# Optimization experiments

Hardware: AMD Instinct MI355X
Metric: run time of the kernel (lower is better)

The kernel has to match this reference:

```python
import jax, jax.numpy as jnp
import numpy as np

N = 100000   # nodes
D = 8        # in_dim/2 (per-node phase dim)
H = 256      # hidden_dim
E = 1600000  # directed edges (avg degree 16)


def setup_inputs() -> dict:
    key = jax.random.key(0)
    ks = jax.random.split(key, 8)
    q = jax.random.normal(ks[0], (N, D), jnp.float32)
    p = jax.random.normal(ks[1], (N, D), jnp.float32)
    # per-node diagonal positive-definite mass matrix (what get_mass() produces:
    # diag(relu(diag(.)) + 1e-4)); keep it well-conditioned for the inverse.
    m_diag = jax.random.uniform(ks[2], (N, D), jnp.float32) + 0.5
    M = jax.vmap(jnp.diag)(m_diag)  # [N, D, D]
    src = jax.random.randint(ks[3], (E,), 0, N, dtype=jnp.int32)
    off = jax.random.randint(ks[4], (E,), 1, N, dtype=jnp.int32)
    dst = ((src + off) % N).astype(jnp.int32)  # guaranteed no self-edges (euclid>0)
    W1 = jax.random.normal(ks[5], (D, H), jnp.float32) / jnp.sqrt(D)
    b1 = jnp.zeros((H,), jnp.float32)
    W2 = jax.random.normal(ks[6], (H, D), jnp.float32) / jnp.sqrt(H)
    b2 = jnp.zeros((D,), jnp.float32)
    gravity = jnp.ones((1, 1), jnp.float32)
    return {"q": q, "p": p, "M": M, "src": src, "dst": dst,
            "W1": W1, "b1": b1, "W2": W2, "b2": b2, "gravity": gravity}


def _gcn(x, src, dst, norm_src, norm_dst, W, b, n_nodes):
    # DGL GraphConv norm='both': D_out^{-1/2} on src, sum-aggregate, D_in^{-1/2} on dst
    m = (x * norm_src[:, None])[src]                       # [E, F]
    agg = jax.ops.segment_sum(m, dst, num_segments=n_nodes)
    return (agg * norm_dst[:, None]) @ W + b


def reference(q, p, M, src, dst, W1, b1, W2, b2, gravity):
    n = q.shape[0]
    ones_e = jnp.ones(src.shape[0], q.dtype)
    out_deg = jax.ops.segment_sum(ones_e, src, num_segments=n)
    in_deg = jax.ops.segment_sum(ones_e, dst, num_segments=n)
    norm_src = jnp.where(out_deg > 0, out_deg, 1.0) ** -0.5
    norm_dst = jnp.where(in_deg > 0, in_deg, 1.0) ** -0.5

    def P_scalar(qq):
        # ConvGNN: GraphConv -> ReLU -> GraphConv, residual add
        h = jax.nn.relu(_gcn(qq, src, dst, norm_src, norm_dst, W1, b1, n))
        h = _gcn(h, src, dst, norm_src, norm_dst, W2, b2, n) + qq      # [N, D]
        euclid = jnp.linalg.norm(h[src] - h[dst], axis=-1)             # [E]
        masses = M[src] * M[dst]                                       # [E, D, D]
        return 0.5 * jnp.sum(gravity[0, 0] * masses / euclid[:, None, None])

    # dHdq = grad of potential P w.r.t q (torch.autograd.grad in original)
    dHdQ = jax.grad(P_scalar)(q)
    # dHdp: per-node p_i @ inv(M_i)  (self-loop graph, degree 1 per node)
    dHdP = jnp.linalg.solve(jnp.swapaxes(M, -1, -2), p[..., None])[..., 0]
    return jnp.concatenate([dHdQ, dHdP], axis=-1)  # [N, 2D]
```

## Files before the change

kernel.cpp:

```cpp
#include <hip/hip_runtime.h>
#include <hip/hip_fp16.h>

#define DD 8
#define HH 256
#define CH 8192
#define PAYBITS 17
#define PAYMASK 0x1FFFF
#define WHPITCH 12


typedef _Float16 h2f __attribute__((ext_vector_type(2)));

static __device__ __forceinline__ float2 u2f(unsigned w) {
    __half2 h = __builtin_bit_cast(__half2, w);
    return __half22float2(h);
}
static __device__ __forceinline__ float dot2u(unsigned w, h2f z, float c) {
#if __has_builtin(__builtin_amdgcn_fdot2)
    return __builtin_amdgcn_fdot2(__builtin_bit_cast(h2f, w), z, c, false);
#else
    float2 f = u2f(w);
    return fmaf(f.y, (float)z[1], fmaf(f.x, (float)z[0], c));
#endif
}
static __device__ __forceinline__ h2f pkh(float a, float b) {
    h2f r; r[0] = (_Float16)a; r[1] = (_Float16)b; return r;
}


__global__ void k_coarse(const int* __restrict__ src, const int* __restrict__ dst,
                         int* __restrict__ gHistIn, int* __restrict__ gHistOut,
                         int NB, int E) {
    __shared__ int hIn[256], hOut[256];
    if (threadIdx.x < 256) { hIn[threadIdx.x] = 0; hOut[threadIdx.x] = 0; }
    __syncthreads();
    int lo = blockIdx.x * CH;
    int hi = min(lo + CH, E);
    for (int i = lo + threadIdx.x; i < hi; i += blockDim.x) {
        atomicAdd(&hIn[dst[i] >> 9], 1);
        atomicAdd(&hOut[src[i] >> 9], 1);
    }
    __syncthreads();
    if (threadIdx.x < NB) {
        int ci = hIn[threadIdx.x], co = hOut[threadIdx.x];
        if (ci) atomicAdd(&gHistIn[threadIdx.x], ci);
        if (co) atomicAdd(&gHistOut[threadIdx.x], co);
    }
}

__global__ void k_cscan(const int* __restrict__ gHistIn, const int* __restrict__ gHistOut,
                        int* __restrict__ cStartIn, int* __restrict__ cStartOut,
                        int* __restrict__ cCurIn, int* __restrict__ cCurOut,
                        int NB, int E) {
    __shared__ int s[256];
#pragma unroll
    for (int dir = 0; dir < 2; dir++) {
        const int* gh = dir ? gHistOut : gHistIn;
        int* cs = dir ? cStartOut : cStartIn;
        int* cc = dir ? cCurOut : cCurIn;
        int v = (threadIdx.x < NB) ? gh[threadIdx.x] : 0;
        s[threadIdx.x] = v;
        __syncthreads();
        for (int off = 1; off < 256; off <<= 1) {
            int t = (threadIdx.x >= off) ? s[threadIdx.x - off] : 0;
            __syncthreads();
            s[threadIdx.x] += t;
            __syncthreads();
        }
        if (threadIdx.x < NB) {
            int ex = s[threadIdx.x] - v;
            cs[threadIdx.x] = ex;
            cc[threadIdx.x] = ex;
        }
        if (threadIdx.x == 0) cs[NB] = E;
        __syncthreads();
    }
}

__global__ void k_part2(const int* __restrict__ src, const int* __restrict__ dst,
                        int* __restrict__ cCurIn, int* __restrict__ cCurOut,
                        int* __restrict__ P_in, int* __restrict__ P_out,
                        int NB, int E) {
    int dir = blockIdx.y;
    const int* key = dir ? src : dst;
    const int* pay = dir ? dst : src;
    int* cCur = dir ? cCurOut : cCurIn;
    int* P    = dir ? P_out   : P_in;
    __shared__ int h[256];
    if (threadIdx.x < 256) h[threadIdx.x] = 0;
    __syncthreads();
    int lo = blockIdx.x * CH;
    int hi = min(lo + CH, E);
    for (int i = lo + threadIdx.x; i < hi; i += blockDim.x)
        atomicAdd(&h[key[i] >> 9], 1);
    __syncthreads();
    if (threadIdx.x < NB) {
        int c = h[threadIdx.x];
        h[threadIdx.x] = c ? atomicAdd(&cCur[threadIdx.x], c) : 0;
    }
    __syncthreads();
    for (int i = lo + threadIdx.x; i < hi; i += blockDim.x) {
        int k = key[i];
        int pos = atomicAdd(&h[k >> 9], 1);
        P[pos] = ((k & 511) << PAYBITS) | pay[i];
    }
}

__launch_bounds__(512)
__global__ void k_fine2(const int* __restrict__ cStartIn, const int* __restrict__ cStartOut,
                        const int* __restrict__ P_in, const int* __restrict__ P_out,
                        int* __restrict__ start_in, int* __restrict__ start_out,
                        int* __restrict__ csr_in, int* __restrict__ csr_out, int N) {
    int dir = blockIdx.y;
    const int* cStart = dir ? cStartOut : cStartIn;
    const int* P      = dir ? P_out     : P_in;
    int* start        = dir ? start_out : start_in;
    int* csr          = dir ? csr_out   : csr_in;
    __shared__ int cnt[512], scn[512];
    int b = blockIdx.x;
    int lo = cStart[b], hi = cStart[b + 1];
    cnt[threadIdx.x] = 0;
    __syncthreads();
    for (int i = lo + threadIdx.x; i < hi; i += 512)
        atomicAdd(&cnt[P[i] >> PAYBITS], 1);
    __syncthreads();
    int own = cnt[threadIdx.x];
    scn[threadIdx.x] = own;
    __syncthreads();
    for (int off = 1; off < 512; off <<= 1) {
        int t = (threadIdx.x >= off) ? scn[threadIdx.x - off] : 0;
        __syncthreads();
        scn[threadIdx.x] += t;
        __syncthreads();
    }
    int base = lo + scn[threadIdx.x] - own;
    int node = (b << 9) + threadIdx.x;
    if (node < N) start[node] = base;
    cnt[threadIdx.x] = base;
    __syncthreads();
    for (int i = lo + threadIdx.x; i < hi; i += 512) {
        int p = P[i];
        int pos = atomicAdd(&cnt[p >> PAYBITS], 1);
        csr[pos] = p & PAYMASK;
    }
}

__global__ void k_prep(const float* __restrict__ q, const float* __restrict__ p,
                       const float* __restrict__ M,
                       const float* __restrict__ W1, const float* __restrict__ W2,
                       unsigned* __restrict__ W12h,
                       int* __restrict__ start_in, int* __restrict__ start_out,
                       float* __restrict__ a, float* __restrict__ b,
                       __half2* __restrict__ hm, __half* __restrict__ qn,
                       float* __restrict__ out, int N, int E) {
    int t = blockIdx.x * blockDim.x + threadIdx.x;
    if (t == 0) { start_in[N] = E; start_out[N] = E; }
    if (t < HH * 8) {
        int j = t >> 3, k = t & 7;
        __half2 hh;
        if (k < 4) {
            hh.x = __float2half(W1[(2 * k) * HH + j]);
            hh.y = __float2half(W1[(2 * k + 1) * HH + j]);
            W12h[j * WHPITCH + k] = *(unsigned*)&hh;
        } else {
            int kk = k - 4;
            hh.x = __float2half(W2[j * DD + 2 * kk]);
            hh.y = __float2half(W2[j * DD + 2 * kk + 1]);
            W12h[j * WHPITCH + 4 + kk] = *(unsigned*)&hh;
        }
    }
    int v = t;
    if (v >= N) return;
    int ei1 = (v + 1 < N) ? start_in[v + 1]  : E;
    int eo1 = (v + 1 < N) ? start_out[v + 1] : E;
    float din  = (float)(ei1 - start_in[v]);
    float dout = (float)(eo1 - start_out[v]);
    float av = 1.0f / sqrtf(dout > 0.f ? dout : 1.f);
    float bv = 1.0f / sqrtf(din  > 0.f ? din  : 1.f);
    a[v] = av; b[v] = bv;
#pragma unroll
    for (int d = 0; d < DD; d++) {
        float m = M[(size_t)v * DD * DD + d * (DD + 1)];
        __half2 hmv;
        hmv.x = __float2half(0.f);
        hmv.y = __float2half(m);
        hm[(size_t)v * DD + d] = hmv;
        qn[(size_t)v * DD + d] = __float2half(av * q[(size_t)v * DD + d]);
        out[(size_t)v * 2 * DD + DD + d] = p[(size_t)v * DD + d] / m;
    }
}

static __device__ __forceinline__
void acc_h8(uint4 r, float acc[8]) {
    float2 f;
    f = __half22float2(*(__half2*)&r.x); acc[0] += f.x; acc[1] += f.y;
    f = __half22float2(*(__half2*)&r.y); acc[2] += f.x; acc[3] += f.y;
    f = __half22float2(*(__half2*)&r.z); acc[4] += f.x; acc[5] += f.y;
    f = __half22float2(*(__half2*)&r.w); acc[6] += f.x; acc[7] += f.y;
}

static __device__ __forceinline__
void unpack_hm(uint4 r0, uint4 r1, float h[8], float m[8]) {
    float2 f;
    f = __half22float2(*(__half2*)&r0.x); h[0] = f.x; m[0] = f.y;
    f = __half22float2(*(__half2*)&r0.y); h[1] = f.x; m[1] = f.y;
    f = __half22float2(*(__half2*)&r0.z); h[2] = f.x; m[2] = f.y;
    f = __half22float2(*(__half2*)&r0.w); h[3] = f.x; m[3] = f.y;
    f = __half22float2(*(__half2*)&r1.x); h[4] = f.x; m[4] = f.y;
    f = __half22float2(*(__half2*)&r1.y); h[5] = f.x; m[5] = f.y;
    f = __half22float2(*(__half2*)&r1.z); h[6] = f.x; m[6] = f.y;
    f = __half22float2(*(__half2*)&r1.w); h[7] = f.x; m[7] = f.y;
}

static __device__ __forceinline__
void gather_h8(const int* __restrict__ csr, const __half* __restrict__ x,
               int e, int e1, float acc[8]) {
    for (; e + 3 < e1; e += 4) {
        int u0 = csr[e], u1 = csr[e + 1], u2 = csr[e + 2], u3 = csr[e + 3];
        uint4 r0 = *(const uint4*)(x + (size_t)u0 * DD);
        uint4 r1 = *(const uint4*)(x + (size_t)u1 * DD);
        uint4 r2 = *(const uint4*)(x + (size_t)u2 * DD);
        uint4 r3 = *(const uint4*)(x + (size_t)u3 * DD);
        acc_h8(r0, acc); acc_h8(r1, acc); acc_h8(r2, acc); acc_h8(r3, acc);
    }
    for (; e < e1; e++) {
        uint4 r = *(const uint4*)(x + (size_t)csr[e] * DD);
        acc_h8(r, acc);
    }
}

__launch_bounds__(256)
__global__ void k_agg_mlp_fwd(const int* __restrict__ start, const int* __restrict__ csr,
                              const __half* __restrict__ qn,
                              const float* __restrict__ a, const float* __restrict__ b,
                              const unsigned* __restrict__ W12h, const float* __restrict__ b1,
                              float* __restrict__ agg1, __half* __restrict__ ya, int N) {
    __shared__ unsigned sWH[HH * WHPITCH];
    __shared__ float sb1[HH];
    for (int i = threadIdx.x; i < HH * WHPITCH; i += 256) sWH[i] = W12h[i];
    for (int i = threadIdx.x; i < HH; i += 256) sb1[i] = b1[i];
    __syncthreads();
    int t = blockIdx.x * 256 + threadIdx.x;
    int v = t >> 4, l16 = t & 15, sub = (t >> 3) & 1, d = t & 7;
    if (v >= N) return;
    int e0 = start[v], e1 = start[v + 1];
    float ag[DD] = {0.f, 0.f, 0.f, 0.f, 0.f, 0.f, 0.f, 0.f};
    for (int e = e0 + l16; e < e1; e += 16) {
        uint4 r = *(const uint4*)(qn + (size_t)csr[e] * DD);
        acc_h8(r, ag);
    }
#pragma unroll
    for (int m = 1; m < 16; m <<= 1)
#pragma unroll
        for (int k = 0; k < DD; k++) ag[k] += __shfl_xor(ag[k], m);
    if (l16 < 2) {
        float4 val = l16 ? make_float4(ag[4], ag[5], ag[6], ag[7])
                         : make_float4(ag[0], ag[1], ag[2], ag[3]);
        ((float4*)(agg1 + (size_t)v * DD))[l16] = val;
    }
    float bv = b[v];
    h2f zh[4];
#pragma unroll
    for (int k = 0; k < 4; k++) zh[k] = pkh(bv * ag[2 * k], bv * ag[2 * k + 1]);
    float acc[DD] = {0.f, 0.f, 0.f, 0.f, 0.f, 0.f, 0.f, 0.f};
    for (int c = 0; c < HH / 16; c += 2) {
        int j0 = (c << 4) | l16, j1 = j0 + 16;
        const uint4* r0 = (const uint4*)(sWH + j0 * WHPITCH);
        const uint4* r1 = (const uint4*)(sWH + j1 * WHPITCH);
        uint4 w1a = r0[0], w2a = r0[1];
        uint4 w1b = r1[0], w2b = r1[1];
        float u0 = sb1[j0], u1 = sb1[j1];
        u0 = dot2u(w1a.x, zh[0], u0); u0 = dot2u(w1a.y, zh[1], u0);
        u0 = dot2u(w1a.z, zh[2], u0); u0 = dot2u(w1a.w, zh[3], u0);
        u1 = dot2u(w1b.x, zh[0], u1); u1 = dot2u(w1b.y, zh[1], u1);
        u1 = dot2u(w1b.z, zh[2], u1); u1 = dot2u(w1b.w, zh[3], u1);
        float h0 = fmaxf(u0, 0.f);
        float h1 = fmaxf(u1, 0.f);
        float2 f;
        f = u2f(w2a.x); acc[0] = fmaf(h0, f.x, acc[0]); acc[1] = fmaf(h0, f.y, acc[1]);
        f = u2f(w2a.y); acc[2] = fmaf(h0, f.x, acc[2]); acc[3] = fmaf(h0, f.y, acc[3]);
        f = u2f(w2a.z); acc[4] = fmaf(h0, f.x, acc[4]); acc[5] = fmaf(h0, f.y, acc[5]);
        f = u2f(w2a.w); acc[6] = fmaf(h0, f.x, acc[6]); acc[7] = fmaf(h0, f.y, acc[7]);
        f = u2f(w2b.x); acc[0] = fmaf(h1, f.x, acc[0]); acc[1] = fmaf(h1, f.y, acc[1]);
        f = u2f(w2b.y); acc[2] = fmaf(h1, f.x, acc[2]); acc[3] = fmaf(h1, f.y, acc[3]);
        f = u2f(w2b.z); acc[4] = fmaf(h1, f.x, acc[4]); acc[5] = fmaf(h1, f.y, acc[5]);
        f = u2f(w2b.w); acc[6] = fmaf(h1, f.x, acc[6]); acc[7] = fmaf(h1, f.y, acc[7]);
    }
#pragma unroll
    for (int m = 1; m < 16; m <<= 1)
#pragma unroll
        for (int k = 0; k < DD; k++) acc[k] += __shfl_xor(acc[k], m);
    float yl = acc[0];
#pragma unroll
    for (int k = 1; k < DD; k++) yl = (d == k) ? acc[k] : yl;
    if (!sub) ya[(size_t)v * DD + d] = __float2half(a[v] * yl);
}

__launch_bounds__(256)
__global__ void k_h_node(const int* __restrict__ start, const int* __restrict__ csr,
                         const __half* __restrict__ ya, const float* __restrict__ b,
                         const float* __restrict__ q, const float* __restrict__ b2,
                         __half2* __restrict__ hm, int N) {
    int t = blockIdx.x * 256 + threadIdx.x;
    int v = t >> 1, half = t & 1;
    if (v >= N) return;
    int e0 = start[v], e1 = start[v + 1];
    int mid = e0 + ((e1 - e0) >> 1);
    float acc[8] = {0.f, 0.f, 0.f, 0.f, 0.f, 0.f, 0.f, 0.f};
    gather_h8(csr, ya, half ? mid : e0, half ? e1 : mid, acc);
#pragma unroll
    for (int k = 0; k < 8; k++) acc[k] += __shfl_xor(acc[k], 1);
    if (!half) {
        float bv = b[v];
        const float4* qp = (const float4*)(q + (size_t)v * DD);
        float4 q0 = qp[0], q1 = qp[1];
        float hq[8] = {q0.x, q0.y, q0.z, q0.w, q1.x, q1.y, q1.z, q1.w};
        __half2* hp = hm + (size_t)v * DD;
#pragma unroll
        for (int k = 0; k < DD; k++) {
            float hval = fmaf(bv, acc[k], b2[k] + hq[k]);
            __half2 cur = hp[k];
            cur.x = __float2half(hval);
            hp[k] = cur;
        }
    }
}

__launch_bounds__(256)
__global__ void k_gh4(const int* __restrict__ start_in, const int* __restrict__ csr_in,
                      const int* __restrict__ start_out, const int* __restrict__ csr_out,
                      const __half2* __restrict__ hm,
                      const float* __restrict__ b, const float* __restrict__ grav,
                      float* __restrict__ gh, __half* __restrict__ bgh, int N) {
    int t = blockIdx.x * 256 + threadIdx.x;
    int v = t >> 2, sub = t & 3, dir = sub >> 1, half = sub & 1;
    if (v >= N) return;
    const uint4* srec = (const uint4*)(hm + (size_t)v * DD);
    uint4 s0 = srec[0], s1 = srec[1];
    float hv[8], mv[8];
    unpack_hm(s0, s1, hv, mv);
    const int* start = dir ? start_out : start_in;
    const int* csr   = dir ? csr_out   : csr_in;
    int e0 = start[v], e1 = start[v + 1];
    int mid = e0 + ((e1 - e0) >> 1);
    int e = half ? mid : e0, hi = half ? e1 : mid;
    float coef = -0.5f * grav[0];
    float acc[8] = {0.f, 0.f, 0.f, 0.f, 0.f, 0.f, 0.f, 0.f};
    for (; e + 1 < hi; e += 2) {
        int u0 = csr[e], u1 = csr[e + 1];
        const uint4* r0p = (const uint4*)(hm + (size_t)u0 * DD);
        const uint4* r1p = (const uint4*)(hm + (size_t)u1 * DD);
        uint4 x0 = r0p[0], x1 = r0p[1], y0 = r1p[0], y1 = r1p[1];
        float hu0[8], mu0[8], hu1[8], mu1[8];
        unpack_hm(x0, x1, hu0, mu0);
        unpack_hm(y0, y1, hu1, mu1);
        float d0[8], d1[8];
        float e20 = 0.f, S0 = 0.f, e21 = 0.f, S1 = 0.f;
#pragma unroll
        for (int k = 0; k < 8; k++) {
            d0[k] = hv[k] - hu0[k];
            d1[k] = hv[k] - hu1[k];
            e20 = fmaf(d0[k], d0[k], e20);
            e21 = fmaf(d1[k], d1[k], e21);
            S0 = fmaf(mv[k], mu0[k], S0);
            S1 = fmaf(mv[k], mu1[k], S1);
        }
        float r0 = rsqrtf(e20), r1 = rsqrtf(e21);
        float c0 = coef * S0 * r0 * r0 * r0;
        float c1 = coef * S1 * r1 * r1 * r1;
#pragma unroll
        for (int k = 0; k < 8; k++)
            acc[k] = fmaf(c0, d0[k], fmaf(c1, d1[k], acc[k]));
    }
    if (e < hi) {
        int u = csr[e];
        const uint4* rp = (const uint4*)(hm + (size_t)u * DD);
        uint4 x0 = rp[0], x1 = rp[1];
        float hu[8], mu[8];
        unpack_hm(x0, x1, hu, mu);
        float df[8];
        float e2 = 0.f, S = 0.f;
#pragma unroll
        for (int k = 0; k < 8; k++) {
            df[k] = hv[k] - hu[k];
            e2 = fmaf(df[k], df[k], e2);
            S = fmaf(mv[k], mu[k], S);
        }
        float r = rsqrtf(e2);
        float c = coef * S * r * r * r;
#pragma unroll
        for (int k = 0; k < 8; k++) acc[k] = fmaf(c, df[k], acc[k]);
    }
#pragma unroll
    for (int k = 0; k < 8; k++) acc[k] += __shfl_xor(acc[k], 1);
#pragma unroll
    for (int k = 0; k < 8; k++) acc[k] += __shfl_xor(acc[k], 2);
    if (sub == 0) {
        float4* gp = (float4*)(gh + (size_t)v * DD);
        gp[0] = make_float4(acc[0], acc[1], acc[2], acc[3]);
        gp[1] = make_float4(acc[4], acc[5], acc[6], acc[7]);
        float bv = b[v];
        __half2* bp = (__half2*)(bgh + (size_t)v * DD);
        bp[0] = __floats2half2_rn(bv * acc[0], bv * acc[1]);
        bp[1] = __floats2half2_rn(bv * acc[2], bv * acc[3]);
        bp[2] = __floats2half2_rn(bv * acc[4], bv * acc[5]);
        bp[3] = __floats2half2_rn(bv * acc[6], bv * acc[7]);
    }
}

__launch_bounds__(256)
__global__ void k_bgh_mlp_bwd(const int* __restrict__ start, const int* __restrict__ csr,
                              const __half* __restrict__ bgh,
                              const float* __restrict__ agg1,
                              const float* __restrict__ a, const float* __restrict__ b,
                              const unsigned* __restrict__ W12h, const float* __restrict__ b1,
                              __half* __restrict__ gz1b, int N) {
    __shared__ unsigned sWH[HH * WHPITCH];
    __shared__ float sb1[HH];
    for (int i = threadIdx.x; i < HH * WHPITCH; i += 256) sWH[i] = W12h[i];
    for (int i = threadIdx.x; i < HH; i += 256) sb1[i] = b1[i];
    __syncthreads();
    int t = blockIdx.x * 256 + threadIdx.x;
    int v = t >> 4, l16 = t & 15, sub = (t >> 3) & 1, d = t & 7;
    if (v >= N) return;
    int e0 = start[v], e1 = start[v + 1];
    float gq[DD] = {0.f, 0.f, 0.f, 0.f, 0.f, 0.f, 0.f, 0.f};
    for (int e = e0 + l16; e < e1; e += 16) {
        uint4 r = *(const uint4*)(bgh + (size_t)csr[e] * DD);
        acc_h8(r, gq);
    }
#pragma unroll
    for (int m = 1; m < 16; m <<= 1)
#pragma unroll
        for (int k = 0; k < DD; k++) gq[k] += __shfl_xor(gq[k], m);
    float bv = b[v], av = a[v];
    float zl = bv * agg1[(size_t)v * DD + d];
    h2f zh[4], gqh[4];
#pragma unroll
    for (int k = 0; k < 4; k++) {
        float za = __shfl(zl, 2 * k, 16), zb = __shfl(zl, 2 * k + 1, 16);
        zh[k] = pkh(za, zb);
        gqh[k] = pkh(gq[2 * k], gq[2 * k + 1]);
    }
    float gz[DD] = {0.f, 0.f, 0.f, 0.f, 0.f, 0.f, 0.f, 0.f};
    for (int c = 0; c < HH / 16; c += 2) {
        int j0 = (c << 4) | l16, j1 = j0 + 16;
        const uint4* r0 = (const uint4*)(sWH + j0 * WHPITCH);
        const uint4* r1 = (const uint4*)(sWH + j1 * WHPITCH);
        uint4 w1a = r0[0], w2a = r0[1];
        uint4 w1b = r1[0], w2b = r1[1];
        float u0 = sb1[j0], u1 = sb1[j1];
        u0 = dot2u(w1a.x, zh[0], u0); u0 = dot2u(w1a.y, zh[1], u0);
        u0 = dot2u(w1a.z, zh[2], u0); u0 = dot2u(w1a.w, zh[3], u0);
        u1 = dot2u(w1b.x, zh[0], u1); u1 = dot2u(w1b.y, zh[1], u1);
        u1 = dot2u(w1b.z, zh[2], u1); u1 = dot2u(w1b.w, zh[3], u1);
        float ga0 = dot2u(w2a.x, gqh[0], 0.f);
        ga0 = dot2u(w2a.y, gqh[1], ga0);
        ga0 = dot2u(w2a.z, gqh[2], ga0);
        ga0 = dot2u(w2a.w, gqh[3], ga0);
        float ga1 = dot2u(w2b.x, gqh[0], 0.f);
        ga1 = dot2u(w2b.y, gqh[1], ga1);
        ga1 = dot2u(w2b.z, gqh[2], ga1);
        ga1 = dot2u(w2b.w, gqh[3], ga1);
        float g0 = (u0 > 0.f) ? av * ga0 : 0.f;
        float g1 = (u1 > 0.f) ? av * ga1 : 0.f;
        float2 f;
        f = u2f(w1a.x); gz[0] = fmaf(g0, f.x, gz[0]); gz[1] = fmaf(g0, f.y, gz[1]);
        f = u2f(w1a.y); gz[2] = fmaf(g0, f.x, gz[2]); gz[3] = fmaf(g0, f.y, gz[3]);
        f = u2f(w1a.z); gz[4] = fmaf(g0, f.x, gz[4]); gz[5] = fmaf(g0, f.y, gz[5]);
        f = u2f(w1a.w); gz[6] = fmaf(g0, f.x, gz[6]); gz[7] = fmaf(g0, f.y, gz[7]);
        f = u2f(w1b.x); gz[0] = fmaf(g1, f.x, gz[0]); gz[1] = fmaf(g1, f.y, gz[1]);
        f = u2f(w1b.y); gz[2] = fmaf(g1, f.x, gz[2]); gz[3] = fmaf(g1, f.y, gz[3]);
        f = u2f(w1b.z); gz[4] = fmaf(g1, f.x, gz[4]); gz[5] = fmaf(g1, f.y, gz[5]);
        f = u2f(w1b.w); gz[6] = fmaf(g1, f.x, gz[6]); gz[7] = fmaf(g1, f.y, gz[7]);
    }
#pragma unroll
    for (int m = 1; m < 16; m <<= 1)
#pragma unroll
        for (int k = 0; k < DD; k++) gz[k] += __shfl_xor(gz[k], m);
    float out_l = gz[0];
#pragma unroll
    for (int k = 1; k < DD; k++) out_l = (d == k) ? gz[k] : out_l;
    if (!sub) gz1b[(size_t)v * DD + d] = __float2half(bv * out_l);
}

__launch_bounds__(256)
__global__ void k_out_node(const int* __restrict__ start, const int* __restrict__ csr,
                           const __half* __restrict__ gz1b, const float* __restrict__ gh,
                           const float* __restrict__ a, float* __restrict__ out, int N) {
    int t = blockIdx.x * 256 + threadIdx.x;
    int v = t >> 1, half = t & 1;
    if (v >= N) return;
    int e0 = start[v], e1 = start[v + 1];
    int mid = e0 + ((e1 - e0) >> 1);
    float acc[8] = {0.f, 0.f, 0.f, 0.f, 0.f, 0.f, 0.f, 0.f};
    gather_h8(csr, gz1b, half ? mid : e0, half ? e1 : mid, acc);
#pragma unroll
    for (int k = 0; k < 8; k++) acc[k] += __shfl_xor(acc[k], 1);
    if (!half) {
        float av = a[v];
        const float4* gp = (const float4*)(gh + (size_t)v * DD);
        float4 g0 = gp[0], g1 = gp[1];
        float4* op = (float4*)(out + (size_t)v * 2 * DD);
        op[0] = make_float4(fmaf(av, acc[0], g0.x), fmaf(av, acc[1], g0.y),
                            fmaf(av, acc[2], g0.z), fmaf(av, acc[3], g0.w));
        op[1] = make_float4(fmaf(av, acc[4], g1.x), fmaf(av, acc[5], g1.y),
                            fmaf(av, acc[6], g1.z), fmaf(av, acc[7], g1.w));
    }
}


extern "C" void kernel_launch(void* const* d_in, const int* in_sizes, int n_in,
                              void* d_out, int out_size, void* d_ws, size_t ws_size,
                              hipStream_t stream) {
    const float* q    = (const float*)d_in[0];
    const float* p    = (const float*)d_in[1];
    const float* M    = (const float*)d_in[2];
    const int*   src  = (const int*)d_in[3];
    const int*   dst  = (const int*)d_in[4];
    const float* W1   = (const float*)d_in[5];
    const float* b1   = (const float*)d_in[6];
    const float* W2   = (const float*)d_in[7];
    const float* b2   = (const float*)d_in[8];
    const float* grav = (const float*)d_in[9];
    float* out = (float*)d_out;

    int N = in_sizes[0] / DD;
    int E = in_sizes[3];
    size_t n = (size_t)N;
    int NB = (N + 511) >> 9;

    float*   ws   = (float*)d_ws;
    float*   a_   = ws;
    float*   b_   = ws + n;
    __half*  qn   = (__half*)(ws + 2 * n);
    float*   agg1 = ws + 10 * n;
    float*   gh   = ws + 18 * n;
    __half2* hm   = (__half2*)(ws + 26 * n);
    __half*  ya   = (__half*)(ws + 34 * n);
    __half*  bgh  = (__half*)(ws + 38 * n);
    __half*  gz1b = (__half*)(ws + 42 * n);

    int* iw        = (int*)(ws + 46 * n);
    int* csr_in    = iw;
    int* csr_out   = iw + (size_t)E;
    int* start_in  = iw + 2 * (size_t)E;
    int* start_out = start_in + n + 1;
    int* gHistIn   = start_out + n + 1;
    int* gHistOut  = gHistIn + 256;
    int* cStartIn  = gHistOut + 256;
    int* cStartOut = cStartIn + NB + 1;
    int* cCurIn    = cStartOut + NB + 1;
    int* cCurOut   = cCurIn + NB;
    int* iwEnd     = cCurOut + NB;
    unsigned* W12h = (unsigned*)iwEnd;
    int* intAfter  = (int*)(W12h + HH * WHPITCH);
    int* P_in  = (E <= 16 * (long long)n) ? (int*)ws            : intAfter;
    int* P_out = (E <= 16 * (long long)n) ? (int*)(ws + 16 * n) : intAfter + E;

    hipMemsetAsync(gHistIn, 0, 512 * sizeof(int), stream);

    const int tb = 256;
    int gbN  = (N + tb - 1) / tb;
    int gb2  = (2 * N + tb - 1) / tb;
    int gb4  = (4 * N + tb - 1) / tb;
    int gb16 = (int)((16 * n + tb - 1) / tb);
    int gbC  = (E + CH - 1) / CH;

    k_coarse  <<<gbC, tb, 0, stream>>>(src, dst, gHistIn, gHistOut, NB, E);
    k_cscan   <<<1, 256, 0, stream>>>(gHistIn, gHistOut, cStartIn, cStartOut,
                                      cCurIn, cCurOut, NB, E);
    k_part2   <<<dim3(gbC, 2), tb, 0, stream>>>(src, dst, cCurIn, cCurOut,
                                                P_in, P_out, NB, E);
    k_fine2   <<<dim3(NB, 2), 512, 0, stream>>>(cStartIn, cStartOut, P_in, P_out,
                                                start_in, start_out, csr_in, csr_out, N);
    k_prep    <<<gbN, tb, 0, stream>>>(q, p, M, W1, W2, W12h, start_in, start_out,
                                       a_, b_, hm, qn, out, N, E);

    k_agg_mlp_fwd<<<gb16, tb, 0, stream>>>(start_in, csr_in, qn, a_, b_,
                                           W12h, b1, agg1, ya, N);
    k_h_node  <<<gb2, tb, 0, stream>>>(start_in, csr_in, ya, b_, q, b2, hm, N);
    k_gh4     <<<gb4, tb, 0, stream>>>(start_in, csr_in, start_out, csr_out,
                                       hm, b_, grav, gh, bgh, N);
    k_bgh_mlp_bwd<<<gb16, tb, 0, stream>>>(start_out, csr_out, bgh, agg1, a_, b_,
                                           W12h, b1, gz1b, N);
    k_out_node<<<gb2, tb, 0, stream>>>(start_out, csr_out, gz1b, gh, a_, out, N);
}
```

Before: 328.5 us.

## Repack MLP weights into per-lane fp16 pairs, use dot2 for second layer and DPP reductions

```diff
diff --git a/kernel.cpp b/kernel.cpp
--- a/kernel.cpp
+++ b/kernel.cpp
@@ -6,25 +6,54 @@
 #define CH 8192
 #define PAYBITS 17
 #define PAYMASK 0x1FFFF
-#define WHPITCH 12
+#define FPITCH 20
+#define BPITCH 28
 
 
 typedef _Float16 h2f __attribute__((ext_vector_type(2)));
 
-static __device__ __forceinline__ float2 u2f(unsigned w) {
-    __half2 h = __builtin_bit_cast(__half2, w);
-    return __half22float2(h);
-}
 static __device__ __forceinline__ float dot2u(unsigned w, h2f z, float c) {
 #if __has_builtin(__builtin_amdgcn_fdot2)
     return __builtin_amdgcn_fdot2(__builtin_bit_cast(h2f, w), z, c, false);
 #else
-    float2 f = u2f(w);
+    __half2 h = __builtin_bit_cast(__half2, w);
+    float2 f = __half22float2(h);
     return fmaf(f.y, (float)z[1], fmaf(f.x, (float)z[0], c));
 #endif
 }
 static __device__ __forceinline__ h2f pkh(float a, float b) {
     h2f r; r[0] = (_Float16)a; r[1] = (_Float16)b; return r;
+}
+static __device__ __forceinline__ unsigned pk2(float a, float b) {
+    __half2 hh; hh.x = __float2half(a); hh.y = __float2half(b);
+    return *(unsigned*)&hh;
+}
+
+template <int CTRL>
+static __device__ __forceinline__ float dppadd(float x) {
+    int y = __builtin_amdgcn_update_dpp(0, __builtin_bit_cast(int, x),
+                                        CTRL, 0xF, 0xF, true);
+    return x + __builtin_bit_cast(float, y);
+}
+static __device__ __forceinline__ void red16(float a[8]) {
+#pragma unroll
+    for (int k = 0; k < 8; k++) a[k] = dppadd<0xB1>(a[k]);
+#pragma unroll
+    for (int k = 0; k < 8; k++) a[k] = dppadd<0x4E>(a[k]);
+#pragma unroll
+    for (int k = 0; k < 8; k++) a[k] = dppadd<0x141>(a[k]);
+#pragma unroll
+    for (int k = 0; k < 8; k++) a[k] = dppadd<0x140>(a[k]);
+}
+static __device__ __forceinline__ void red2(float a[8]) {
+#pragma unroll
+    for (int k = 0; k < 8; k++) a[k] = dppadd<0xB1>(a[k]);
+}
+static __device__ __forceinline__ void red4(float a[8]) {
+#pragma unroll
+    for (int k = 0; k < 8; k++) a[k] = dppadd<0xB1>(a[k]);
+#pragma unroll
+    for (int k = 0; k < 8; k++) a[k] = dppadd<0x4E>(a[k]);
 }
 
 
@@ -148,26 +177,36 @@
 __global__ void k_prep(const float* __restrict__ q, const float* __restrict__ p,
                        const float* __restrict__ M,
                        const float* __restrict__ W1, const float* __restrict__ W2,
-                       unsigned* __restrict__ W12h,
+                       unsigned* __restrict__ Fp, unsigned* __restrict__ Bp,
                        int* __restrict__ start_in, int* __restrict__ start_out,
                        float* __restrict__ a, float* __restrict__ b,
                        __half2* __restrict__ hm, __half* __restrict__ qn,
                        float* __restrict__ out, int N, int E) {
     int t = blockIdx.x * blockDim.x + threadIdx.x;
     if (t == 0) { start_in[N] = E; start_out[N] = E; }
-    if (t < HH * 8) {
-        int j = t >> 3, k = t & 7;
-        __half2 hh;
-        if (k < 4) {
-            hh.x = __float2half(W1[(2 * k) * HH + j]);
-            hh.y = __float2half(W1[(2 * k + 1) * HH + j]);
-            W12h[j * WHPITCH + k] = *(unsigned*)&hh;
-        } else {
-            int kk = k - 4;
-            hh.x = __float2half(W2[j * DD + 2 * kk]);
-            hh.y = __float2half(W2[j * DD + 2 * kk + 1]);
-            W12h[j * WHPITCH + 4 + kk] = *(unsigned*)&hh;
+    if (t < 128) {
+        int ci = t >> 4, l16 = t & 15;
+        int j0 = ci * 32 + l16, j1 = j0 + 16;
+        unsigned* F = Fp + t * FPITCH;
+        unsigned* B = Bp + t * BPITCH;
+#pragma unroll
+        for (int k = 0; k < 4; k++) {
+            unsigned c0 = pk2(W1[(2 * k) * HH + j0], W1[(2 * k + 1) * HH + j0]);
+            unsigned c1 = pk2(W1[(2 * k) * HH + j1], W1[(2 * k + 1) * HH + j1]);
+            F[k] = c0; F[4 + k] = c1; B[k] = c0; B[4 + k] = c1;
         }
+#pragma unroll
+        for (int k = 0; k < 8; k++)
+            F[8 + k] = pk2(W2[j0 * DD + k], W2[j1 * DD + k]);
+#pragma unroll
+        for (int kk = 0; kk < 4; kk++) {
+            B[8 + kk]  = pk2(W2[j0 * DD + 2 * kk], W2[j0 * DD + 2 * kk + 1]);
+            B[12 + kk] = pk2(W2[j1 * DD + 2 * kk], W2[j1 * DD + 2 * kk + 1]);
+        }
+#pragma unroll
+        for (int d = 0; d < 8; d++)
+            B[16 + d] = pk2(W1[d * HH + j0], W1[d * HH + j1]);
+        B[24] = 0; B[25] = 0; B[26] = 0; B[27] = 0;
     }
     int v = t;
     if (v >= N) return;
@@ -233,11 +272,11 @@
 __global__ void k_agg_mlp_fwd(const int* __restrict__ start, const int* __restrict__ csr,
                               const __half* __restrict__ qn,
                               const float* __restrict__ a, const float* __restrict__ b,
-                              const unsigned* __restrict__ W12h, const float* __restrict__ b1,
+                              const unsigned* __restrict__ Fp, const float* __restrict__ b1,
                               float* __restrict__ agg1, __half* __restrict__ ya, int N) {
-    __shared__ unsigned sWH[HH * WHPITCH];
+    __shared__ unsigned sF[128 * FPITCH];
     __shared__ float sb1[HH];
-    for (int i = threadIdx.x; i < HH * WHPITCH; i += 256) sWH[i] = W12h[i];
+    for (int i = threadIdx.x; i < 128 * FPITCH; i += 256) sF[i] = Fp[i];
     for (int i = threadIdx.x; i < HH; i += 256) sb1[i] = b1[i];
     __syncthreads();
     int t = blockIdx.x * 256 + threadIdx.x;
@@ -249,10 +288,7 @@
         uint4 r = *(const uint4*)(qn + (size_t)csr[e] * DD);
         acc_h8(r, ag);
     }
-#pragma unroll
-    for (int m = 1; m < 16; m <<= 1)
-#pragma unroll
-        for (int k = 0; k < DD; k++) ag[k] += __shfl_xor(ag[k], m);
+    red16(ag);
     if (l16 < 2) {
         float4 val = l16 ? make_float4(ag[4], ag[5], ag[6], ag[7])
                          : make_float4(ag[0], ag[1], ag[2], ag[3]);
@@ -263,33 +299,24 @@
 #pragma unroll
     for (int k = 0; k < 4; k++) zh[k] = pkh(bv * ag[2 * k], bv * ag[2 * k + 1]);
     float acc[DD] = {0.f, 0.f, 0.f, 0.f, 0.f, 0.f, 0.f, 0.f};
-    for (int c = 0; c < HH / 16; c += 2) {
-        int j0 = (c << 4) | l16, j1 = j0 + 16;
-        const uint4* r0 = (const uint4*)(sWH + j0 * WHPITCH);
-        const uint4* r1 = (const uint4*)(sWH + j1 * WHPITCH);
-        uint4 w1a = r0[0], w2a = r0[1];
-        uint4 w1b = r1[0], w2b = r1[1];
-        float u0 = sb1[j0], u1 = sb1[j1];
+#pragma unroll
+    for (int ci = 0; ci < 8; ci++) {
+        int pid = ci * 16 + l16;
+        const uint4* pw = (const uint4*)(sF + pid * FPITCH);
+        uint4 w1a = pw[0], w1b = pw[1], w2p0 = pw[2], w2p1 = pw[3];
+        int j0 = ci * 32 + l16;
+        float u0 = sb1[j0], u1 = sb1[j0 + 16];
         u0 = dot2u(w1a.x, zh[0], u0); u0 = dot2u(w1a.y, zh[1], u0);
         u0 = dot2u(w1a.z, zh[2], u0); u0 = dot2u(w1a.w, zh[3], u0);
         u1 = dot2u(w1b.x, zh[0], u1); u1 = dot2u(w1b.y, zh[1], u1);
         u1 = dot2u(w1b.z, zh[2], u1); u1 = dot2u(w1b.w, zh[3], u1);
-        float h0 = fmaxf(u0, 0.f);
-        float h1 = fmaxf(u1, 0.f);
-        float2 f;
-        f = u2f(w2a.x); acc[0] = fmaf(h0, f.x, acc[0]); acc[1] = fmaf(h0, f.y, acc[1]);
-        f = u2f(w2a.y); acc[2] = fmaf(h0, f.x, acc[2]); acc[3] = fmaf(h0, f.y, acc[3]);
-        f = u2f(w2a.z); acc[4] = fmaf(h0, f.x, acc[4]); acc[5] = fmaf(h0, f.y, acc[5]);
-        f = u2f(w2a.w); acc[6] = fmaf(h0, f.x, acc[6]); acc[7] = fmaf(h0, f.y, acc[7]);
-        f = u2f(w2b.x); acc[0] = fmaf(h1, f.x, acc[0]); acc[1] = fmaf(h1, f.y, acc[1]);
-        f = u2f(w2b.y); acc[2] = fmaf(h1, f.x, acc[2]); acc[3] = fmaf(h1, f.y, acc[3]);
-        f = u2f(w2b.z); acc[4] = fmaf(h1, f.x, acc[4]); acc[5] = fmaf(h1, f.y, acc[5]);
-        f = u2f(w2b.w); acc[6] = fmaf(h1, f.x, acc[6]); acc[7] = fmaf(h1, f.y, acc[7]);
-    }
-#pragma unroll
-    for (int m = 1; m < 16; m <<= 1)
-#pragma unroll
-        for (int k = 0; k < DD; k++) acc[k] += __shfl_xor(acc[k], m);
+        h2f hh = pkh(fmaxf(u0, 0.f), fmaxf(u1, 0.f));
+        acc[0] = dot2u(w2p0.x, hh, acc[0]); acc[1] = dot2u(w2p0.y, hh, acc[1]);
+        acc[2] = dot2u(w2p0.z, hh, acc[2]); acc[3] = dot2u(w2p0.w, hh, acc[3]);
+        acc[4] = dot2u(w2p1.x, hh, acc[4]); acc[5] = dot2u(w2p1.y, hh, acc[5]);
+        acc[6] = dot2u(w2p1.z, hh, acc[6]); acc[7] = dot2u(w2p1.w, hh, acc[7]);
+    }
+    red16(acc);
     float yl = acc[0];
 #pragma unroll
     for (int k = 1; k < DD; k++) yl = (d == k) ? acc[k] : yl;
@@ -308,8 +335,7 @@
     int mid = e0 + ((e1 - e0) >> 1);
     float acc[8] = {0.f, 0.f, 0.f, 0.f, 0.f, 0.f, 0.f, 0.f};
     gather_h8(csr, ya, half ? mid : e0, half ? e1 : mid, acc);
-#pragma unroll
-    for (int k = 0; k < 8; k++) acc[k] += __shfl_xor(acc[k], 1);
+    red2(acc);
     if (!half) {
         float bv = b[v];
         const float4* qp = (const float4*)(q + (size_t)v * DD);
@@ -391,10 +417,7 @@
 #pragma unroll
         for (int k = 0; k < 8; k++) acc[k] = fmaf(c, df[k], acc[k]);
     }
-#pragma unroll
-    for (int k = 0; k < 8; k++) acc[k] += __shfl_xor(acc[k], 1);
-#pragma unroll
-    for (int k = 0; k < 8; k++) acc[k] += __shfl_xor(acc[k], 2);
+    red4(acc);
     if (sub == 0) {
         float4* gp = (float4*)(gh + (size_t)v * DD);
         gp[0] = make_float4(acc[0], acc[1], acc[2], acc[3]);
@@ -413,11 +436,11 @@
                               const __half* __restrict__ bgh,
                               const float* __restrict__ agg1,
                               const float* __restrict__ a, const float* __restrict__ b,
-                              const unsigned* __restrict__ W12h, const float* __restrict__ b1,
+                              const unsigned* __restrict__ Bp, const float* __restrict__ b1,
                               __half* __restrict__ gz1b, int N) {
-    __shared__ unsigned sWH[HH * WHPITCH];
+    __shared__ unsigned sB[128 * BPITCH];
     __shared__ float sb1[HH];
-    for (int i = threadIdx.x; i < HH * WHPITCH; i += 256) sWH[i] = W12h[i];
+    for (int i = threadIdx.x; i < 128 * BPITCH; i += 256) sB[i] = Bp[i];
     for (int i = threadIdx.x; i < HH; i += 256) sb1[i] = b1[i];
     __syncthreads();
     int t = blockIdx.x * 256 + threadIdx.x;
@@ -429,55 +452,45 @@
         uint4 r = *(const uint4*)(bgh + (size_t)csr[e] * DD);
         acc_h8(r, gq);
     }
-#pragma unroll
-    for (int m = 1; m < 16; m <<= 1)
-#pragma unroll
-        for (int k = 0; k < DD; k++) gq[k] += __shfl_xor(gq[k], m);
+    red16(gq);
     float bv = b[v], av = a[v];
-    float zl = bv * agg1[(size_t)v * DD + d];
+    const float4* ap = (const float4*)(agg1 + (size_t)v * DD);
+    float4 a0 = ap[0], a1 = ap[1];
     h2f zh[4], gqh[4];
-#pragma unroll
-    for (int k = 0; k < 4; k++) {
-        float za = __shfl(zl, 2 * k, 16), zb = __shfl(zl, 2 * k + 1, 16);
-        zh[k] = pkh(za, zb);
-        gqh[k] = pkh(gq[2 * k], gq[2 * k + 1]);
-    }
+    zh[0] = pkh(bv * a0.x, bv * a0.y); zh[1] = pkh(bv * a0.z, bv * a0.w);
+    zh[2] = pkh(bv * a1.x, bv * a1.y); zh[3] = pkh(bv * a1.z, bv * a1.w);
+#pragma unroll
+    for (int k = 0; k < 4; k++) gqh[k] = pkh(gq[2 * k], gq[2 * k + 1]);
     float gz[DD] = {0.f, 0.f, 0.f, 0.f, 0.f, 0.f, 0.f, 0.f};
-    for (int c = 0; c < HH / 16; c += 2) {
-        int j0 = (c << 4) | l16, j1 = j0 + 16;
-        const uint4* r0 = (const uint4*)(sWH + j0 * WHPITCH);
-        const uint4* r1 = (const uint4*)(sWH + j1 * WHPITCH);
-        uint4 w1a = r0[0], w2a = r0[1];
-        uint4 w1b = r1[0], w2b = r1[1];
-        float u0 = sb1[j0], u1 = sb1[j1];
+#pragma unroll
+    for (int ci = 0; ci < 8; ci++) {
+        int pid = ci * 16 + l16;
+        const uint4* pw = (const uint4*)(sB + pid * BPITCH);
+        uint4 w1a = pw[0], w1b = pw[1], w2r0 = pw[2], w2r1 = pw[3];
+        uint4 g0p = pw[4], g1p = pw[5];
+        int j0 = ci * 32 + l16;
+        float u0 = sb1[j0], u1 = sb1[j0 + 16];
         u0 = dot2u(w1a.x, zh[0], u0); u0 = dot2u(w1a.y, zh[1], u0);
         u0 = dot2u(w1a.z, zh[2], u0); u0 = dot2u(w1a.w, zh[3], u0);
         u1 = dot2u(w1b.x, zh[0], u1); u1 = dot2u(w1b.y, zh[1], u1);
         u1 = dot2u(w1b.z, zh[2], u1); u1 = dot2u(w1b.w, zh[3], u1);
-        float ga0 = dot2u(w2a.x, gqh[0], 0.f);
-        ga0 = dot2u(w2a.y, gqh[1], ga0);
-        ga0 = dot2u(w2a.z, gqh[2], ga0);
-        ga0 = dot2u(w2a.w, gqh[3], ga0);
-        float ga1 = dot2u(w2b.x, gqh[0], 0.f);
-        ga1 = dot2u(w2b.y, gqh[1], ga1);
-        ga1 = dot2u(w2b.z, gqh[2], ga1);
-        ga1 = dot2u(w2b.w, gqh[3], ga1);
+        float ga0 = dot2u(w2r0.x, gqh[0], 0.f);
+        ga0 = dot2u(w2r0.y, gqh[1], ga0);
+        ga0 = dot2u(w2r0.z, gqh[2], ga0);
+        ga0 = dot2u(w2r0.w, gqh[3], ga0);
+        float ga1 = dot2u(w2r1.x, gqh[0], 0.f);
+        ga1 = dot2u(w2r1.y, gqh[1], ga1);
+        ga1 = dot2u(w2r1.z, gqh[2], ga1);
+        ga1 = dot2u(w2r1.w, gqh[3], ga1);
         float g0 = (u0 > 0.f) ? av * ga0 : 0.f;
         float g1 = (u1 > 0.f) ? av * ga1 : 0.f;
-        float2 f;
-        f = u2f(w1a.x); gz[0] = fmaf(g0, f.x, gz[0]); gz[1] = fmaf(g0, f.y, gz[1]);
-        f = u2f(w1a.y); gz[2] = fmaf(g0, f.x, gz[2]); gz[3] = fmaf(g0, f.y, gz[3]);
-        f = u2f(w1a.z); gz[4] = fmaf(g0, f.x, gz[4]); gz[5] = fmaf(g0, f.y, gz[5]);
-        f = u2f(w1a.w); gz[6] = fmaf(g0, f.x, gz[6]); gz[7] = fmaf(g0, f.y, gz[7]);
-        f = u2f(w1b.x); gz[0] = fmaf(g1, f.x, gz[0]); gz[1] = fmaf(g1, f.y, gz[1]);
-        f = u2f(w1b.y); gz[2] = fmaf(g1, f.x, gz[2]); gz[3] = fmaf(g1, f.y, gz[3]);
-        f = u2f(w1b.z); gz[4] = fmaf(g1, f.x, gz[4]); gz[5] = fmaf(g1, f.y, gz[5]);
-        f = u2f(w1b.w); gz[6] = fmaf(g1, f.x, gz[6]); gz[7] = fmaf(g1, f.y, gz[7]);
-    }
-#pragma unroll
-    for (int m = 1; m < 16; m <<= 1)
-#pragma unroll
-        for (int k = 0; k < DD; k++) gz[k] += __shfl_xor(gz[k], m);
+        h2f gg = pkh(g0, g1);
+        gz[0] = dot2u(g0p.x, gg, gz[0]); gz[1] = dot2u(g0p.y, gg, gz[1]);
+        gz[2] = dot2u(g0p.z, gg, gz[2]); gz[3] = dot2u(g0p.w, gg, gz[3]);
+        gz[4] = dot2u(g1p.x, gg, gz[4]); gz[5] = dot2u(g1p.y, gg, gz[5]);
+        gz[6] = dot2u(g1p.z, gg, gz[6]); gz[7] = dot2u(g1p.w, gg, gz[7]);
+    }
+    red16(gz);
     float out_l = gz[0];
 #pragma unroll
     for (int k = 1; k < DD; k++) out_l = (d == k) ? gz[k] : out_l;
@@ -495,8 +508,7 @@
     int mid = e0 + ((e1 - e0) >> 1);
     float acc[8] = {0.f, 0.f, 0.f, 0.f, 0.f, 0.f, 0.f, 0.f};
     gather_h8(csr, gz1b, half ? mid : e0, half ? e1 : mid, acc);
-#pragma unroll
-    for (int k = 0; k < 8; k++) acc[k] += __shfl_xor(acc[k], 1);
+    red2(acc);
     if (!half) {
         float av = a[v];
         const float4* gp = (const float4*)(gh + (size_t)v * DD);
@@ -553,8 +565,9 @@
     int* cCurIn    = cStartOut + NB + 1;
     int* cCurOut   = cCurIn + NB;
     int* iwEnd     = cCurOut + NB;
-    unsigned* W12h = (unsigned*)iwEnd;
-    int* intAfter  = (int*)(W12h + HH * WHPITCH);
+    unsigned* Fp   = (unsigned*)iwEnd;
+    unsigned* Bp   = Fp + 128 * FPITCH;
+    int* intAfter  = (int*)(Bp + 128 * BPITCH);
     int* P_in  = (E <= 16 * (long long)n) ? (int*)ws            : intAfter;
     int* P_out = (E <= 16 * (long long)n) ? (int*)(ws + 16 * n) : intAfter + E;
 
@@ -574,15 +587,15 @@
                                                 P_in, P_out, NB, E);
     k_fine2   <<<dim3(NB, 2), 512, 0, stream>>>(cStartIn, cStartOut, P_in, P_out,
                                                 start_in, start_out, csr_in, csr_out, N);
-    k_prep    <<<gbN, tb, 0, stream>>>(q, p, M, W1, W2, W12h, start_in, start_out,
+    k_prep    <<<gbN, tb, 0, stream>>>(q, p, M, W1, W2, Fp, Bp, start_in, start_out,
                                        a_, b_, hm, qn, out, N, E);
 
     k_agg_mlp_fwd<<<gb16, tb, 0, stream>>>(start_in, csr_in, qn, a_, b_,
-                                           W12h, b1, agg1, ya, N);
+                                           Fp, b1, agg1, ya, N);
     k_h_node  <<<gb2, tb, 0, stream>>>(start_in, csr_in, ya, b_, q, b2, hm, N);
     k_gh4     <<<gb4, tb, 0, stream>>>(start_in, csr_in, start_out, csr_out,
                                        hm, b_, grav, gh, bgh, N);
     k_bgh_mlp_bwd<<<gb16, tb, 0, stream>>>(start_out, csr_out, bgh, agg1, a_, b_,
-                                           W12h, b1, gz1b, N);
+                                           Bp, b1, gz1b, N);
     k_out_node<<<gb2, tb, 0, stream>>>(start_out, csr_out, gz1b, gh, a_, out, N);
 }
```

New measurement: 311.7 us. 1.05x faster.
